# Performance work log

Hardware: AMD Instinct MI355X
Metric: run time of the kernel (lower is better)

## Reference

```python
import jax, jax.numpy as jnp
import numpy as np

B, N, K, F_IN, F_OUT = 2, 196608, 9, 64, 64


def setup_inputs() -> dict:
    key = jax.random.key(0)
    k1, k2, k3 = jax.random.split(key, 3)
    x = jax.random.normal(k1, (B, N, F_IN), dtype=jnp.float32)
    adjc = jax.random.randint(k2, (N, K), 0, N, dtype=jnp.int64)
    # first neighbor is the cell itself (typical grid adjacency)
    adjc = adjc.at[:, 0].set(jnp.arange(N, dtype=jnp.int64))
    scale = 1.0 / np.sqrt(K * F_IN)
    W = jax.random.normal(k3, (K, F_IN, F_OUT), dtype=jnp.float32) * scale
    b = jnp.zeros((F_OUT,), dtype=jnp.float32)
    return {"x": x, "adjc": adjc, "W": W, "b": b}


def reference(x, adjc, W, b):
    # get_nh: irregular gather of neighbor features -> [B, N, K, F_in]
    x_nh = x[:, adjc, :]
    # learned layer: contract over (neighborhood, in_features) -> [B, N, F_out]
    out = jnp.einsum("bnkf,kfo->bno", x_nh, W) + b
    return out
```

## Files before the change

kernel.cpp:

```cpp
#include <hip/hip_runtime.h>

#define B_ 2
#define N_ 196608
#define K_ 9
#define F_ 64
#define ROWS 64
#define ROWB 256

typedef __attribute__((ext_vector_type(8))) short short8;
typedef __attribute__((ext_vector_type(8))) unsigned short ushort8;
typedef __attribute__((ext_vector_type(4))) float f32x4;

__device__ __forceinline__ unsigned short f2bf(float f) {
  unsigned u = __builtin_bit_cast(unsigned, f);
  u = (u + 0x7fffu + ((u >> 16) & 1u)) >> 16;
  return (unsigned short)u;
}

__global__ __launch_bounds__(256) void cvt_x_kernel(const float* __restrict__ x,
                                                    unsigned short* __restrict__ xb) {
  const long i = (long)blockIdx.x * 256 + threadIdx.x;
  const long n = i >> 3;
  const int b = (int)((i >> 2) & 1);
  const int q4 = (int)(i & 3);
  const float4* src = (const float4*)(x + ((size_t)b * N_ + n) * F_ + q4 * 16);
  float4 v[4];
#pragma unroll
  for (int j = 0; j < 4; ++j) v[j] = src[j];
  ushort8 r0, r1;
  r0[0] = f2bf(v[0].x); r0[1] = f2bf(v[0].y); r0[2] = f2bf(v[0].z); r0[3] = f2bf(v[0].w);
  r0[4] = f2bf(v[1].x); r0[5] = f2bf(v[1].y); r0[6] = f2bf(v[1].z); r0[7] = f2bf(v[1].w);
  r1[0] = f2bf(v[2].x); r1[1] = f2bf(v[2].y); r1[2] = f2bf(v[2].z); r1[3] = f2bf(v[2].w);
  r1[4] = f2bf(v[3].x); r1[5] = f2bf(v[3].y); r1[6] = f2bf(v[3].z); r1[7] = f2bf(v[3].w);
  ushort8* dst = (ushort8*)(xb + ((size_t)n * 2 + b) * F_ + q4 * 16);
  dst[0] = r0;
  dst[1] = r1;
}

__global__ __launch_bounds__(256) void cvt_w_kernel(const float* __restrict__ W,
                                                    unsigned short* __restrict__ wt) {
  const int i = blockIdx.x * 256 + threadIdx.x;
  const int k = i >> 12;
  const int rem = i & 4095;
  const int o = rem >> 6;
  const int f = rem & 63;
  wt[i] = f2bf(W[(k << 12) + (f << 6) + o]);
}

__global__ __launch_bounds__(256, 3) void nhconv_main(
    const short* __restrict__ xb,
    const int* __restrict__ adjc,
    const short* __restrict__ wt,
    const float* __restrict__ bias,
    float* __restrict__ out) {
  __shared__ short abuf[2][ROWS * 128];
  __shared__ int s_adj[ROWS * K_];

  const int tid = (int)threadIdx.x;
  const int n0 = blockIdx.x * ROWS;

  for (int i = tid; i < ROWS * K_; i += 256)
    s_adj[i] = __builtin_nontemporal_load(adjc + (size_t)n0 * K_ + i);
  __syncthreads();

  const int w = tid >> 6;
  const int l = tid & 63;
  const int q = l >> 4;
  const int c = l & 15;

  auto stage = [&](int k, int bf) {
#pragma unroll
    for (int j = 0; j < 4; ++j) {
      const int row = w * 16 + j * 4 + (l >> 4);
      const int src_chunk = (l & 15) ^ (row & 7);
      const size_t goff = (size_t)(unsigned)s_adj[row * K_ + k] * ROWB + (src_chunk << 4);
      const char* src = (const char*)xb + goff;
      short* dst = &abuf[bf][(w * 16 + j * 4) * 128];
      __builtin_amdgcn_global_load_lds(
          (const __attribute__((address_space(1))) unsigned int*)src,
          (__attribute__((address_space(3))) unsigned int*)dst, 16, 0, 0);
    }
  };

  f32x4 acc[2][4];
#pragma unroll
  for (int p = 0; p < 2; ++p)
#pragma unroll
    for (int ct = 0; ct < 4; ++ct)
      acc[p][ct] = (f32x4){0.f, 0.f, 0.f, 0.f};

  stage(0, 0);

  for (int k = 0; k < K_; ++k) {
    __syncthreads();
    if (k + 1 < K_) stage(k + 1, (k + 1) & 1);

    const short* bufk = abuf[k & 1];
    const int arow = (w * 16 + c) * 128;
#pragma unroll
    for (int fs = 0; fs < 2; ++fs) {
      const int ch0 = (fs * 4 + q) ^ (c & 7);
      const int ch1 = (8 + fs * 4 + q) ^ (c & 7);
      const short8 a0 = *(const short8*)&bufk[arow + (ch0 << 3)];
      const short8 a1 = *(const short8*)&bufk[arow + (ch1 << 3)];
      const short* wk = wt + (k << 12) + fs * 32 + q * 8 + (c << 6);
#pragma unroll
      for (int ct = 0; ct < 4; ++ct) {
        const short8 bf = *(const short8*)(wk + (ct << 10));
        acc[0][ct] = __builtin_amdgcn_mfma_f32_16x16x32_bf16(a0, bf, acc[0][ct], 0, 0, 0);
        acc[1][ct] = __builtin_amdgcn_mfma_f32_16x16x32_bf16(a1, bf, acc[1][ct], 0, 0, 0);
      }
    }
  }

  float bv[4];
#pragma unroll
  for (int ct = 0; ct < 4; ++ct) bv[ct] = bias[ct * 16 + c];

#pragma unroll
  for (int p = 0; p < 2; ++p) {
    const size_t outbase = ((size_t)p * N_ + (size_t)(n0 + w * 16)) * F_;
#pragma unroll
    for (int ct = 0; ct < 4; ++ct) {
#pragma unroll
      for (int rr = 0; rr < 4; ++rr) {
        const int row = q * 4 + rr;
        __builtin_nontemporal_store(acc[p][ct][rr] + bv[ct],
                                    &out[outbase + (size_t)row * F_ + ct * 16 + c]);
      }
    }
  }
}

extern "C" void kernel_launch(void* const* d_in, const int* in_sizes, int n_in,
                              void* d_out, int out_size, void* d_ws, size_t ws_size,
                              hipStream_t stream) {
  const float* x = (const float*)d_in[0];
  const int* adjc = (const int*)d_in[1];
  const float* W = (const float*)d_in[2];
  const float* bias = (const float*)d_in[3];
  float* out = (float*)d_out;

  unsigned short* xb = (unsigned short*)d_ws;
  unsigned short* wt = (unsigned short*)((char*)d_ws + (size_t)B_ * N_ * F_ * 2);

  cvt_x_kernel<<<6144, 256, 0, stream>>>(x, xb);
  cvt_w_kernel<<<144, 256, 0, stream>>>(W, wt);

  nhconv_main<<<N_ / ROWS, 256, 0, stream>>>((const short*)xb, adjc, (const short*)wt,
                                             bias, out);
}
```

Measured before the change: 310.0 us.

## Triple-buffer neighbor gathers with per-wave sync and register-prefetched weights

The main kernel moves from double to triple LDS buffering, staging gathers two neighbors ahead. It replaces the per-iteration __syncthreads with explicit vmcnt/lgkmcnt waits, relying on each wave loading only its own rows and adjacency entries. Weight fragments are prefetched into registers one step ahead instead of being loaded from global memory right before the MFMAs. The x conversion kernel is also reshaped to one float4 per thread with a 2D grid. The changes add LDS and register pressure, and they depend on hand-tuned waitcnt values being correct.

```diff
diff --git a/kernel.cpp b/kernel.cpp
--- a/kernel.cpp
+++ b/kernel.cpp
@@ -8,7 +8,7 @@
 #define ROWB 256
 
 typedef __attribute__((ext_vector_type(8))) short short8;
-typedef __attribute__((ext_vector_type(8))) unsigned short ushort8;
+typedef __attribute__((ext_vector_type(4))) unsigned short ushort4v;
 typedef __attribute__((ext_vector_type(4))) float f32x4;
 
 __device__ __forceinline__ unsigned short f2bf(float f) {
@@ -19,22 +19,14 @@
 
 __global__ __launch_bounds__(256) void cvt_x_kernel(const float* __restrict__ x,
                                                     unsigned short* __restrict__ xb) {
-  const long i = (long)blockIdx.x * 256 + threadIdx.x;
-  const long n = i >> 3;
-  const int b = (int)((i >> 2) & 1);
-  const int q4 = (int)(i & 3);
-  const float4* src = (const float4*)(x + ((size_t)b * N_ + n) * F_ + q4 * 16);
-  float4 v[4];
-#pragma unroll
-  for (int j = 0; j < 4; ++j) v[j] = src[j];
-  ushort8 r0, r1;
-  r0[0] = f2bf(v[0].x); r0[1] = f2bf(v[0].y); r0[2] = f2bf(v[0].z); r0[3] = f2bf(v[0].w);
-  r0[4] = f2bf(v[1].x); r0[5] = f2bf(v[1].y); r0[6] = f2bf(v[1].z); r0[7] = f2bf(v[1].w);
-  r1[0] = f2bf(v[2].x); r1[1] = f2bf(v[2].y); r1[2] = f2bf(v[2].z); r1[3] = f2bf(v[2].w);
-  r1[4] = f2bf(v[3].x); r1[5] = f2bf(v[3].y); r1[6] = f2bf(v[3].z); r1[7] = f2bf(v[3].w);
-  ushort8* dst = (ushort8*)(xb + ((size_t)n * 2 + b) * F_ + q4 * 16);
-  dst[0] = r0;
-  dst[1] = r1;
+  const int b = blockIdx.y;
+  const long cidx = (long)blockIdx.x * 256 + threadIdx.x;
+  const long n = cidx >> 4;
+  const int qd = (int)(cidx & 15);
+  const float4 v = *(const float4*)(x + ((size_t)b * N_ + n) * F_ + (size_t)qd * 4);
+  ushort4v r;
+  r[0] = f2bf(v.x); r[1] = f2bf(v.y); r[2] = f2bf(v.z); r[3] = f2bf(v.w);
+  *(ushort4v*)(xb + ((size_t)n * 2 + b) * F_ + qd * 4) = r;
 }
 
 __global__ __launch_bounds__(256) void cvt_w_kernel(const float* __restrict__ W,
@@ -53,20 +45,22 @@
     const short* __restrict__ wt,
     const float* __restrict__ bias,
     float* __restrict__ out) {
-  __shared__ short abuf[2][ROWS * 128];
+  __shared__ short abuf[3][ROWS * 128];
   __shared__ int s_adj[ROWS * K_];
 
   const int tid = (int)threadIdx.x;
   const int n0 = blockIdx.x * ROWS;
-
-  for (int i = tid; i < ROWS * K_; i += 256)
-    s_adj[i] = __builtin_nontemporal_load(adjc + (size_t)n0 * K_ + i);
-  __syncthreads();
-
   const int w = tid >> 6;
   const int l = tid & 63;
   const int q = l >> 4;
   const int c = l & 15;
+
+  {
+    const int base = w * (16 * K_);
+    for (int i = l; i < 16 * K_; i += 64)
+      s_adj[base + i] =
+          __builtin_nontemporal_load(adjc + (size_t)(n0 + w * 16) * K_ + i);
+  }
 
   auto stage = [&](int k, int bf) {
 #pragma unroll
@@ -82,6 +76,16 @@
     }
   };
 
+  const short* wbase = wt + q * 8 + (c << 6);
+  short8 rw[2][8];
+  auto wload = [&](int k, int par) {
+#pragma unroll
+    for (int fs = 0; fs < 2; ++fs)
+#pragma unroll
+      for (int ct = 0; ct < 4; ++ct)
+        rw[par][fs * 4 + ct] = *(const short8*)(wbase + (k << 12) + fs * 32 + (ct << 10));
+  };
+
   f32x4 acc[2][4];
 #pragma unroll
   for (int p = 0; p < 2; ++p)
@@ -89,13 +93,27 @@
     for (int ct = 0; ct < 4; ++ct)
       acc[p][ct] = (f32x4){0.f, 0.f, 0.f, 0.f};
 
+  wload(0, 0);
   stage(0, 0);
+  wload(1, 1);
+  stage(1, 1);
 
+#pragma unroll
   for (int k = 0; k < K_; ++k) {
-    __syncthreads();
-    if (k + 1 < K_) stage(k + 1, (k + 1) & 1);
+    asm volatile("s_waitcnt lgkmcnt(0)" ::: "memory");
+    if (k >= 1 && k + 1 < K_) wload(k + 1, (k + 1) & 1);
+    if (k + 2 < K_) stage(k + 2, (k + 2) % 3);
 
-    const short* bufk = abuf[k & 1];
+    if (k <= K_ - 3) {
+      asm volatile("s_waitcnt vmcnt(16)" ::: "memory");
+    } else if (k == K_ - 2) {
+      asm volatile("s_waitcnt vmcnt(12)" ::: "memory");
+    } else {
+      asm volatile("s_waitcnt vmcnt(0)" ::: "memory");
+    }
+    __builtin_amdgcn_sched_barrier(0);
+
+    const short* bufk = abuf[k % 3];
     const int arow = (w * 16 + c) * 128;
 #pragma unroll
     for (int fs = 0; fs < 2; ++fs) {
@@ -103,12 +121,11 @@
       const int ch1 = (8 + fs * 4 + q) ^ (c & 7);
       const short8 a0 = *(const short8*)&bufk[arow + (ch0 << 3)];
       const short8 a1 = *(const short8*)&bufk[arow + (ch1 << 3)];
-      const short* wk = wt + (k << 12) + fs * 32 + q * 8 + (c << 6);
 #pragma unroll
       for (int ct = 0; ct < 4; ++ct) {
-        const short8 bf = *(const short8*)(wk + (ct << 10));
-        acc[0][ct] = __builtin_amdgcn_mfma_f32_16x16x32_bf16(a0, bf, acc[0][ct], 0, 0, 0);
-        acc[1][ct] = __builtin_amdgcn_mfma_f32_16x16x32_bf16(a1, bf, acc[1][ct], 0, 0, 0);
+        const short8 bfr = rw[k & 1][fs * 4 + ct];
+        acc[0][ct] = __builtin_amdgcn_mfma_f32_16x16x32_bf16(a0, bfr, acc[0][ct], 0, 0, 0);
+        acc[1][ct] = __builtin_amdgcn_mfma_f32_16x16x32_bf16(a1, bfr, acc[1][ct], 0, 0, 0);
       }
     }
   }
@@ -144,7 +161,7 @@
   unsigned short* xb = (unsigned short*)d_ws;
   unsigned short* wt = (unsigned short*)((char*)d_ws + (size_t)B_ * N_ * F_ * 2);
 
-  cvt_x_kernel<<<6144, 256, 0, stream>>>(x, xb);
+  cvt_x_kernel<<<dim3(N_ * 16 / 256, B_), 256, 0, stream>>>(x, xb);
   cvt_w_kernel<<<144, 256, 0, stream>>>(W, wt);
 
   nhconv_main<<<N_ / ROWS, 256, 0, stream>>>((const short*)xb, adjc, (const short*)wt,
```

Measured after the change: 297.4 us. 4.1% less time.
